# Optimization experiments

Hardware: AMD Instinct MI355X
Metric: run time of the kernel (lower is better)

The kernel has to match this reference:

```python
import jax, jax.numpy as jnp
import numpy as np

# --- static CT geometry (shapes must be static under jit; mirrors the `options` vector) ---
B = 8          # batch
V = 720        # number of projection views
D = 736        # detector bins per view
H = 512        # image height (pixels)
W = 512        # image width  (pixels)
DIMG = 0.006641            # image pixel size (physical units)
DDET = 0.0066              # detector bin size
ANG0 = 0.0                 # starting angle
DANG = 2.0 * np.pi / V     # angular step


def setup_inputs() -> dict:
    key = jax.random.key(0)
    proj = jax.random.normal(key, (B, 1, V, D), dtype=jnp.float32)
    options = jnp.array(
        [V, D, W, H, DIMG, DDET, ANG0, DANG, 5.95, 4.906, 0.0, 2.0],
        dtype=jnp.float32,
    )
    return {"proj": proj, "options": options}


def _backproject(sino):
    """Pixel-driven parallel-beam back-projection of one sinogram [V, D] -> image [H, W]."""
    xs = (jnp.arange(W, dtype=jnp.float32) - (W - 1) / 2.0) * DIMG   # pixel-center x
    ys = ((H - 1) / 2.0 - jnp.arange(H, dtype=jnp.float32)) * DIMG   # pixel-center y
    x = jnp.broadcast_to(xs[None, :], (H, W))
    y = jnp.broadcast_to(ys[:, None], (H, W))
    angles = ANG0 + jnp.arange(V, dtype=jnp.float32) * DANG

    def body(acc, inp):
        ang, row = inp                               # row: [D] detector samples at this view
        t = x * jnp.cos(ang) + y * jnp.sin(ang)      # ray coordinate of each pixel
        u = t / DDET + (D - 1) / 2.0                 # fractional detector index
        u0 = jnp.floor(u)
        w = u - u0
        i0 = u0.astype(jnp.int32)
        i1 = i0 + 1
        v0 = jnp.where((i0 >= 0) & (i0 < D), row[jnp.clip(i0, 0, D - 1)], 0.0)
        v1 = jnp.where((i1 >= 0) & (i1 < D), row[jnp.clip(i1, 0, D - 1)], 0.0)
        return acc + (1.0 - w) * v0 + w * v1, None

    acc, _ = jax.lax.scan(body, jnp.zeros((H, W), jnp.float32), (angles, sino))
    return acc * DANG  # angular integration weight


def reference(proj, options):
    # `options` carries the geometry; its shape-determining entries are baked in statically.
    sino = proj.reshape(B, V, D)
    img = jax.vmap(_backproject)(sino)
    return img.reshape(B, 1, H, W)
```

## Files before the change

### kernel.cpp

```cpp
#include <hip/hip_runtime.h>

#define BATCH 8
#define NVIEW 720
#define NPAIR 360
#define NGRP  180
#define NDET  736
#define IMGH  512
#define IMGW  512

#define DANG_F  ((float)(6.283185307179586 / 720.0))
#define RATIO_F ((float)(0.006641 / 0.0066))
#define UCENTER ((float)((NDET - 1) * 0.5))

#define PADDET 768
#define NITER  90
#define ITER_BYTES 12288
#define WS_BYTES ((size_t)BATCH * NITER * PADDET * 16)

typedef float  v2f __attribute__((ext_vector_type(2)));
typedef __fp16 v2h __attribute__((ext_vector_type(2)));
typedef __fp16 v8h __attribute__((ext_vector_type(8)));

struct alignas(16) E16 { v2h ag, bg, am, bm; };

__device__ __forceinline__ void fuse5(const float* __restrict__ fwd,
                                      const float* __restrict__ rev,
                                      int i, float s[5]) {
    const float4 f4 = *(const float4*)(fwd + i);
    const float  f1 = fwd[i + 4];
    const float4 r4 = *(const float4*)(rev + (732 - i));
    const float  r1 = rev[731 - i];
    s[0] = f4.x + r4.w; s[1] = f4.y + r4.z; s[2] = f4.z + r4.y;
    s[3] = f4.w + r4.x; s[4] = f1 + r1;
}

__global__ __launch_bounds__(192) void prep_kernel(
    const float* __restrict__ proj, E16* __restrict__ ws)
{
    const int t = threadIdx.x;
    if (t >= 184) return;
    const int p = blockIdx.x;
    const int b = blockIdx.y;
    const int g = (p < 89) ? p + 1   : 0;
    const int m = (p < 89) ? 179 - p : 90;
    const int i = 4 * t;
    const float* __restrict__ base = proj + (size_t)b * NVIEW * NDET;
    float sAg[5], sBg[5], sAm[5], sBm[5];
    fuse5(base + (size_t)g * NDET,         base + (size_t)(g + 360) * NDET, i, sAg);
    fuse5(base + (size_t)(g + 180) * NDET, base + (size_t)(g + 540) * NDET, i, sBg);
    fuse5(base + (size_t)m * NDET,         base + (size_t)(m + 360) * NDET, i, sAm);
    fuse5(base + (size_t)(m + 180) * NDET, base + (size_t)(m + 540) * NDET, i, sBm);
    E16* __restrict__ dst = ws + ((size_t)b * NITER + p) * PADDET + i;
#pragma unroll
    for (int k = 0; k < 4; ++k) {
        E16 e;
        e.ag = __builtin_amdgcn_cvt_pkrtz(sAg[k + 1] - sAg[k], sAg[k]);
        e.bg = __builtin_amdgcn_cvt_pkrtz(sBg[k + 1] - sBg[k], sBg[k]);
        e.am = __builtin_amdgcn_cvt_pkrtz(sAm[k + 1] - sAm[k], sAm[k]);
        e.bm = __builtin_amdgcn_cvt_pkrtz(sBm[k + 1] - sBm[k], sBm[k]);
        dst[k] = e;
    }
}

#define VIS(Lp, u, r0, r1, r2, r3) do {                                      \
    const float uu_ = (u);                                                   \
    const int   ii_ = (int)uu_;                                              \
    const v2h wv_ = __builtin_amdgcn_cvt_pkrtz(                              \
        __builtin_amdgcn_fractf(uu_), 1.0f);                                 \
    const v8h E_ = (Lp)[ii_];                                                \
    r0 = __builtin_amdgcn_fdot2((v2h){E_[0], E_[1]}, wv_, r0, false);        \
    r1 = __builtin_amdgcn_fdot2((v2h){E_[2], E_[3]}, wv_, r1, false);        \
    r2 = __builtin_amdgcn_fdot2((v2h){E_[4], E_[5]}, wv_, r2, false);        \
    r3 = __builtin_amdgcn_fdot2((v2h){E_[6], E_[7]}, wv_, r3, false);        \
} while (0)

#define VIS2(Lp, O, u, p0, p1, q0, q1) do {                                  \
    const float uu_ = (u);                                                   \
    const int   ii_ = (int)uu_;                                              \
    const v2h wv_ = __builtin_amdgcn_cvt_pkrtz(                              \
        __builtin_amdgcn_fractf(uu_), 1.0f);                                 \
    const v8h E_ = (Lp)[ii_];                                                \
    const v2h ha_ = {E_[(O)], E_[(O) + 1]};                                  \
    const v2h hb_ = {E_[(O) + 2], E_[(O) + 3]};                              \
    p0 = __builtin_amdgcn_fdot2(ha_, wv_, p0, false);                        \
    p1 = __builtin_amdgcn_fdot2(ha_, wv_, p1, false);                        \
    q0 = __builtin_amdgcn_fdot2(hb_, wv_, q0, false);                        \
    q1 = __builtin_amdgcn_fdot2(hb_, wv_, q1, false);                        \
} while (0)

#define VIS1(Lp, O, u, p0, q0) do {                                          \
    const float uu_ = (u);                                                   \
    const int   ii_ = (int)uu_;                                              \
    const v2h wv_ = __builtin_amdgcn_cvt_pkrtz(                              \
        __builtin_amdgcn_fractf(uu_), 1.0f);                                 \
    const v8h E_ = (Lp)[ii_];                                                \
    p0 = __builtin_amdgcn_fdot2((v2h){E_[(O)], E_[(O) + 1]}, wv_, p0, false);\
    q0 = __builtin_amdgcn_fdot2((v2h){E_[(O) + 2], E_[(O) + 3]}, wv_, q0,    \
                                false);                                      \
} while (0)

__global__ __launch_bounds__(512, 4) void backproject_dma_kernel(
    const v8h* __restrict__ ws, float* __restrict__ out)
{
    __shared__ alignas(16) v8h lds4[4][PADDET];
    __shared__ v2f cs[NGRP];

    const int tid  = threadIdx.x;
    const int wave = tid >> 6;
    const int lane = tid & 63;

    if (tid < NGRP) {
        float s, c;
        sincosf((float)tid * DANG_F, &s, &c);
        cs[tid] = (v2f){c * RATIO_F, s * RATIO_F};
    }

    const int b = blockIdx.z;
    const int h = (int)blockIdx.y * 8 + wave;
    const int w = (int)blockIdx.x * 64 + lane;

    const bool dg = (w == h);
    const bool rm = (w > h);
    const int  H  = rm ? 255 - h : h;
    const int  W  = rm ? 255 - w : w;

    const float px  = (float)W - 255.5f;
    const float py  = 255.5f - (float)H;
    const float px2 = dg ? (-0.5f - (float)W) : py;
    const float py2 = dg ? ( 0.5f + (float)H) : px;

    const char* __restrict__ wsb =
        (const char*)(ws + (size_t)b * NITER * PADDET);

    float A0 = 0.f, A1 = 0.f, A2 = 0.f, A3 = 0.f;
    float B0 = 0.f, B1 = 0.f, B2 = 0.f, B3 = 0.f;
    float X0 = 0.f, X1 = 0.f, X2 = 0.f, X3 = 0.f;
    float Y0 = 0.f, Y1 = 0.f, Y2 = 0.f, Y3 = 0.f;

    auto issue = [&](int p) {
        const char* g0 = wsb + (size_t)p * ITER_BYTES;
        char* l0 = (char*)&lds4[p & 3][0];
        __builtin_amdgcn_global_load_lds(
            (const __attribute__((address_space(1))) void*)
                (g0 + wave * 1024 + lane * 16),
            (__attribute__((address_space(3))) void*)(l0 + wave * 1024),
            16, 0, 0);
        if (wave < 4) {
            const int s = 8 + wave;
            __builtin_amdgcn_global_load_lds(
                (const __attribute__((address_space(1))) void*)
                    (g0 + s * 1024 + lane * 16),
                (__attribute__((address_space(3))) void*)(l0 + s * 1024),
                16, 0, 0);
        }
    };

    issue(0);
    __syncthreads();

    const v2f cc = {UCENTER, UCENTER};
    for (int p = 0; p < NITER - 1; ++p) {
        issue(p + 1);
        {
            const v8h* __restrict__ L = &lds4[p & 3][0];
            const v2f t  = cs[p + 1];
            const v2f m1 = {t.x, -t.y};
            const v2f m2 = {t.y, t.x};
            const v2f gA = __builtin_elementwise_fma(
                (v2f){px, px}, m1, (v2f){py, py} * m2);
            const v2f gB = __builtin_elementwise_fma(
                (v2f){px2, px2}, m1, (v2f){py2, py2} * m2);
            const v2f upA = cc + gA, umA = cc - gA;
            const v2f upB = cc + gB, umB = cc - gB;
            VIS(L, upA.x, A0, A1, X2, X3);
            VIS(L, umA.x, A2, A3, X0, X1);
            VIS(L, upA.y, A3, A0, X3, X0);
            VIS(L, umA.y, A1, A2, X1, X2);
            VIS(L, upB.x, B2, B3, Y0, Y1);
            VIS(L, umB.x, B0, B1, Y2, Y3);
            VIS(L, upB.y, B1, B2, Y1, Y2);
            VIS(L, umB.y, B3, B0, Y3, Y0);
        }
        __syncthreads();
    }

    {
        const v8h* __restrict__ L = &lds4[(NITER - 1) & 3][0];
        const v2f t0 = cs[0], t45 = cs[90];
        if (!dg) {
            const float g1 = px * t0.x + py * t0.y;
            const float g2 = -px * t0.y + py * t0.x;
            VIS2(L, 0, UCENTER + g1, A0, X1, A1, X2);
            VIS2(L, 0, UCENTER - g1, A2, X3, A3, X0);
            VIS2(L, 0, UCENTER + g2, A3, X2, A0, X3);
            VIS2(L, 0, UCENTER - g2, A1, X0, A2, X1);
            const float h1 = px * t45.x + py * t45.y;
            const float h2 = -px * t45.y + py * t45.x;
            VIS2(L, 4, UCENTER + h1, A0, X2, A1, X3);
            VIS2(L, 4, UCENTER - h1, A2, X0, A3, X1);
            VIS2(L, 4, UCENTER + h2, A3, X3, A0, X0);
            VIS2(L, 4, UCENTER - h2, A1, X1, A2, X2);
        } else {
            const float g1  = px * t0.x + py * t0.y;
            const float g1b = px2 * t0.x + py2 * t0.y;
            VIS2(L, 0, UCENTER + g1,  A0, A1, A1, A2);
            VIS2(L, 0, UCENTER - g1,  A2, A3, A0, A3);
            VIS2(L, 0, UCENTER + g1b, B2, B3, B3, B0);
            VIS2(L, 0, UCENTER - g1b, B0, B1, B2, B1);
            {
                const v2h wv_ = __builtin_amdgcn_cvt_pkrtz(0.5f, 1.0f);
                const v8h E_ = L[(int)UCENTER];
                const v2h ha_ = {E_[4], E_[5]};
                const v2h hb_ = {E_[6], E_[7]};
                A0 = __builtin_amdgcn_fdot2(ha_, wv_, A0, false);
                A2 = __builtin_amdgcn_fdot2(ha_, wv_, A2, false);
                B2 = __builtin_amdgcn_fdot2(ha_, wv_, B2, false);
                B0 = __builtin_amdgcn_fdot2(ha_, wv_, B0, false);
                A1 = __builtin_amdgcn_fdot2(hb_, wv_, A1, false);
                A3 = __builtin_amdgcn_fdot2(hb_, wv_, A3, false);
                B3 = __builtin_amdgcn_fdot2(hb_, wv_, B3, false);
                B1 = __builtin_amdgcn_fdot2(hb_, wv_, B1, false);
            }
            const float e1 = (px + px) * t45.x;
            const float e2 = (px2 + px2) * t45.x;
            VIS1(L, 4, UCENTER + e1, A1, A2);
            VIS1(L, 4, UCENTER - e1, A3, A0);
            VIS1(L, 4, UCENTER + e2, B3, B0);
            VIS1(L, 4, UCENTER - e2, B1, B2);
        }
    }

    const float aE0 = dg ? X0 : Y0, aE1 = dg ? X1 : Y1;
    const float aE2 = dg ? X2 : Y2, aE3 = dg ? X3 : Y3;
    const float bE0 = dg ? Y0 : X0, bE1 = dg ? Y1 : X1;
    const float bE2 = dg ? Y2 : X2, bE3 = dg ? Y3 : X3;
    const float a0 = (A0 + aE0) * DANG_F, a1 = (A1 + aE1) * DANG_F;
    const float a2 = (A2 + aE2) * DANG_F, a3 = (A3 + aE3) * DANG_F;
    const float b0 = (B0 + bE0) * DANG_F, b1 = (B1 + bE1) * DANG_F;
    const float b2 = (B2 + bE2) * DANG_F, b3 = (B3 + bE3) * DANG_F;

    float* __restrict__ o = out + (size_t)b * IMGH * IMGW;
    const int Qr = dg ? 256 + H : W;
    const int Qc = dg ? 256 + W : H;
    o[H * IMGW + W]                         = a0;
    o[(511 - W) * IMGW + H]                 = a1;
    o[(511 - H) * IMGW + (511 - W)]         = a2;
    o[W * IMGW + (511 - H)]                 = a3;
    o[Qr * IMGW + Qc]                       = b0;
    o[(511 - Qc) * IMGW + Qr]               = b1;
    o[(511 - Qr) * IMGW + (511 - Qc)]       = b2;
    o[Qc * IMGW + (511 - Qr)]               = b3;
}

struct Stage { float4 f4, r4; float f1, r1; };

__device__ __forceinline__ void fb_load(const float* __restrict__ sino,
                                        int k, int t, Stage& S) {
    if (t < 368) {
        const int p  = (t >= 184);
        const int i  = 4 * (t - 184 * p);
        const int vf = k + 180 * p;
        const float* __restrict__ fwd = sino + vf * NDET;
        const float* __restrict__ rev = sino + (vf + NPAIR) * NDET;
        S.f4 = *(const float4*)(fwd + i);
        S.f1 = fwd[i + 4];
        S.r4 = *(const float4*)(rev + (732 - i));
        S.r1 = rev[731 - i];
    }
}

__device__ __forceinline__ void fb_write(v2h* __restrict__ L, int t,
                                         const Stage& S) {
    if (t < 368) {
        const int p = (t >= 184);
        const int i = 4 * (t - 184 * p);
        const float s0 = S.f4.x + S.r4.w;
        const float s1 = S.f4.y + S.r4.z;
        const float s2 = S.f4.z + S.r4.y;
        const float s3 = S.f4.w + S.r4.x;
        const float s4 = S.f1 + S.r1;
        const v2h n0 = __builtin_amdgcn_cvt_pkrtz(s1 - s0, s0);
        const v2h n1 = __builtin_amdgcn_cvt_pkrtz(s2 - s1, s1);
        const v2h n2 = __builtin_amdgcn_cvt_pkrtz(s3 - s2, s2);
        const v2h n3 = __builtin_amdgcn_cvt_pkrtz(s4 - s3, s3);
        struct alignas(16) H4 { v2h a, b, c, d; };
        *(H4*)(L + p * NDET + i) = H4{n0, n1, n2, n3};
    }
}

__device__ __forceinline__ void fb_visit(const v2h* __restrict__ L,
                                         float u, float& accA, float& accB) {
    const int   i0 = (int)u;
    const float fr = __builtin_amdgcn_fractf(u);
    const v2h wv = __builtin_amdgcn_cvt_pkrtz(fr, 1.0f);
    const v2h A = L[i0];
    const v2h B = L[i0 + NDET];
    accA = __builtin_amdgcn_fdot2(A, wv, accA, false);
    accB = __builtin_amdgcn_fdot2(B, wv, accB, false);
}

__global__ __launch_bounds__(512, 4) void backproject_fb_kernel(
    const float* __restrict__ proj, float* __restrict__ out)
{
    __shared__ alignas(16) v2h lds[2][2][2 * NDET];
    __shared__ v2f cs[NGRP];

    const int tid = threadIdx.x;
    if (tid < NGRP) {
        float s, c;
        sincosf((float)tid * DANG_F, &s, &c);
        cs[tid] = (v2f){c * RATIO_F, s * RATIO_F};
    }

    const int b    = blockIdx.z;
    const int lane = tid & 63;
    const int h    = (int)blockIdx.y * 8 + (tid >> 6);
    const int w0   = (int)blockIdx.x * 64 + lane;

    const float px = (float)w0 - (float)(IMGW - 1) * 0.5f;
    const float py = (float)(IMGH - 1) * 0.5f - (float)h;

    const float* __restrict__ sino = proj + (size_t)b * NVIEW * NDET;

    float a0 = 0.f, a1 = 0.f, a2 = 0.f, a3 = 0.f;
    float b0 = 0.f, b1 = 0.f, b2 = 0.f, b3 = 0.f;

    Stage s0 = {}, s1 = {};
    fb_load(sino, 0, tid, s0);
    fb_load(sino, 1, tid, s1);
    fb_write(lds[0][0], tid, s0);
    fb_write(lds[0][1], tid, s1);
    fb_load(sino, 2, tid, s0);
    fb_load(sino, 3, tid, s1);
    __syncthreads();

    for (int gg = 0; gg < NGRP; gg += 2) {
        const int buf = (gg >> 1) & 1;
#pragma unroll
        for (int sub = 0; sub < 2; ++sub) {
            const v2h* __restrict__ L = lds[buf][sub];
            const v2f t = cs[gg + sub];
            const v2f m1 = {t.x, -t.y};
            const v2f m2 = {t.y, t.x};
            const v2f pxv = {px, px};
            const v2f pyv = {py, py};
            const v2f gvec = __builtin_elementwise_fma(pxv, m1, pyv * m2);
            const v2f cc = {UCENTER, UCENTER};
            const v2f up = cc + gvec;
            const v2f um = cc - gvec;
            const v2f dd = {128.0f, 128.0f};
            const v2f dm = dd * m1;
            const v2f vp = up + dm;
            const v2f vm = um - dm;

            fb_visit(L, up.x, a0, a1);
            fb_visit(L, um.x, a2, a3);
            fb_visit(L, up.y, a3, a0);
            fb_visit(L, um.y, a1, a2);
            fb_visit(L, vp.x, b0, b1);
            fb_visit(L, vm.x, b2, b3);
            fb_visit(L, vp.y, b3, b0);
            fb_visit(L, vm.y, b1, b2);
        }
        if (gg < NGRP - 2) {
            fb_write(lds[buf ^ 1][0], tid, s0);
            fb_write(lds[buf ^ 1][1], tid, s1);
            if (gg < NGRP - 4) {
                fb_load(sino, gg + 4, tid, s0);
                fb_load(sino, gg + 5, tid, s1);
            }
            __syncthreads();
        }
    }

    float* __restrict__ o = out + (size_t)b * IMGH * IMGW;
    const int hm  = (IMGH - 1) - h;
    const int w1  = w0 + 128;
    const int wm0 = (IMGW - 1) - w0;
    const int wm1 = (IMGW - 1) - w1;
    o[h   * IMGW + w0 ] = a0 * DANG_F;
    o[wm0 * IMGW + h  ] = a1 * DANG_F;
    o[hm  * IMGW + wm0] = a2 * DANG_F;
    o[w0  * IMGW + hm ] = a3 * DANG_F;
    o[h   * IMGW + w1 ] = b0 * DANG_F;
    o[wm1 * IMGW + h  ] = b1 * DANG_F;
    o[hm  * IMGW + wm1] = b2 * DANG_F;
    o[w1  * IMGW + hm ] = b3 * DANG_F;
}

extern "C" void kernel_launch(void* const* d_in, const int* in_sizes, int n_in,
                              void* d_out, int out_size, void* d_ws, size_t ws_size,
                              hipStream_t stream) {
    const float* proj = (const float*)d_in[0];
    float* out = (float*)d_out;

    if (ws_size >= WS_BYTES) {
        E16* ws = (E16*)d_ws;
        prep_kernel<<<dim3(NITER, BATCH), 192, 0, stream>>>(proj, ws);
        backproject_dma_kernel<<<dim3(2, 32, BATCH), 512, 0, stream>>>(
            (const v8h*)ws, out);
    } else {
        backproject_fb_kernel<<<dim3(2, 32, BATCH), 512, 0, stream>>>(proj, out);
    }
}
```

Baseline: 144.7 us.

## Swizzle LDS detector layout, interleave batch in block order, double-step DMA loop

Stores the preprocessed detector entries in an XOR-swizzled order so that gathered LDS reads from neighbouring pixels fall into different banks, with the swizzle applied in both the prep writes and every LDS lookup. Block indices are remapped so that consecutive blocks walk across batch images instead of tiles, changing L2 and cache locality. The main loop now processes two angle groups per barrier and issues two DMA prefetches ahead, halving the number of __syncthreads. The added index arithmetic and deeper prefetch use extra VALU work and depend on the 4-slot LDS ring staying consistent.

```diff
diff --git a/kernel.cpp b/kernel.cpp
--- a/kernel.cpp
+++ b/kernel.cpp
@@ -16,6 +16,8 @@
 #define NITER  90
 #define ITER_BYTES 12288
 #define WS_BYTES ((size_t)BATCH * NITER * PADDET * 16)
+
+#define SWZ(j) ((j) ^ (((j) >> 3) & 7))
 
 typedef float  v2f __attribute__((ext_vector_type(2)));
 typedef __fp16 v2h __attribute__((ext_vector_type(2)));
@@ -39,8 +41,9 @@
 {
     const int t = threadIdx.x;
     if (t >= 184) return;
-    const int p = blockIdx.x;
-    const int b = blockIdx.y;
+    const int flat = (int)blockIdx.y * 90 + (int)blockIdx.x;
+    const int b = flat & 7;
+    const int p = flat >> 3;
     const int g = (p < 89) ? p + 1   : 0;
     const int m = (p < 89) ? 179 - p : 90;
     const int i = 4 * t;
@@ -50,7 +53,7 @@
     fuse5(base + (size_t)(g + 180) * NDET, base + (size_t)(g + 540) * NDET, i, sBg);
     fuse5(base + (size_t)m * NDET,         base + (size_t)(m + 360) * NDET, i, sAm);
     fuse5(base + (size_t)(m + 180) * NDET, base + (size_t)(m + 540) * NDET, i, sBm);
-    E16* __restrict__ dst = ws + ((size_t)b * NITER + p) * PADDET + i;
+    E16* __restrict__ dstb = ws + ((size_t)b * NITER + p) * PADDET;
 #pragma unroll
     for (int k = 0; k < 4; ++k) {
         E16 e;
@@ -58,7 +61,8 @@
         e.bg = __builtin_amdgcn_cvt_pkrtz(sBg[k + 1] - sBg[k], sBg[k]);
         e.am = __builtin_amdgcn_cvt_pkrtz(sAm[k + 1] - sAm[k], sAm[k]);
         e.bm = __builtin_amdgcn_cvt_pkrtz(sBm[k + 1] - sBm[k], sBm[k]);
-        dst[k] = e;
+        const int j = i + k;
+        dstb[SWZ(j)] = e;
     }
 }
 
@@ -67,7 +71,7 @@
     const int   ii_ = (int)uu_;                                              \
     const v2h wv_ = __builtin_amdgcn_cvt_pkrtz(                              \
         __builtin_amdgcn_fractf(uu_), 1.0f);                                 \
-    const v8h E_ = (Lp)[ii_];                                                \
+    const v8h E_ = (Lp)[SWZ(ii_)];                                           \
     r0 = __builtin_amdgcn_fdot2((v2h){E_[0], E_[1]}, wv_, r0, false);        \
     r1 = __builtin_amdgcn_fdot2((v2h){E_[2], E_[3]}, wv_, r1, false);        \
     r2 = __builtin_amdgcn_fdot2((v2h){E_[4], E_[5]}, wv_, r2, false);        \
@@ -79,7 +83,7 @@
     const int   ii_ = (int)uu_;                                              \
     const v2h wv_ = __builtin_amdgcn_cvt_pkrtz(                              \
         __builtin_amdgcn_fractf(uu_), 1.0f);                                 \
-    const v8h E_ = (Lp)[ii_];                                                \
+    const v8h E_ = (Lp)[SWZ(ii_)];                                           \
     const v2h ha_ = {E_[(O)], E_[(O) + 1]};                                  \
     const v2h hb_ = {E_[(O) + 2], E_[(O) + 3]};                              \
     p0 = __builtin_amdgcn_fdot2(ha_, wv_, p0, false);                        \
@@ -93,7 +97,7 @@
     const int   ii_ = (int)uu_;                                              \
     const v2h wv_ = __builtin_amdgcn_cvt_pkrtz(                              \
         __builtin_amdgcn_fractf(uu_), 1.0f);                                 \
-    const v8h E_ = (Lp)[ii_];                                                \
+    const v8h E_ = (Lp)[SWZ(ii_)];                                           \
     p0 = __builtin_amdgcn_fdot2((v2h){E_[(O)], E_[(O) + 1]}, wv_, p0, false);\
     q0 = __builtin_amdgcn_fdot2((v2h){E_[(O) + 2], E_[(O) + 3]}, wv_, q0,    \
                                 false);                                      \
@@ -115,9 +119,12 @@
         cs[tid] = (v2f){c * RATIO_F, s * RATIO_F};
     }
 
-    const int b = blockIdx.z;
-    const int h = (int)blockIdx.y * 8 + wave;
-    const int w = (int)blockIdx.x * 64 + lane;
+    const int flat = ((int)blockIdx.z * 32 + (int)blockIdx.y) * 2
+                     + (int)blockIdx.x;
+    const int b    = flat & 7;
+    const int tile = flat >> 3;
+    const int h = (tile >> 1) * 8 + wave;
+    const int w = (tile & 1) * 64 + lane;
 
     const bool dg = (w == h);
     const bool rm = (w > h);
@@ -155,37 +162,43 @@
         }
     };
 
+    const v2f cc = {UCENTER, UCENTER};
+    auto groups = [&](int p) {
+        const v8h* __restrict__ L = &lds4[p & 3][0];
+        const v2f t  = cs[p + 1];
+        const v2f m1 = {t.x, -t.y};
+        const v2f m2 = {t.y, t.x};
+        const v2f gA = __builtin_elementwise_fma(
+            (v2f){px, px}, m1, (v2f){py, py} * m2);
+        const v2f gB = __builtin_elementwise_fma(
+            (v2f){px2, px2}, m1, (v2f){py2, py2} * m2);
+        const v2f upA = cc + gA, umA = cc - gA;
+        const v2f upB = cc + gB, umB = cc - gB;
+        VIS(L, upA.x, A0, A1, X2, X3);
+        VIS(L, umA.x, A2, A3, X0, X1);
+        VIS(L, upA.y, A3, A0, X3, X0);
+        VIS(L, umA.y, A1, A2, X1, X2);
+        VIS(L, upB.x, B2, B3, Y0, Y1);
+        VIS(L, umB.x, B0, B1, Y2, Y3);
+        VIS(L, upB.y, B1, B2, Y1, Y2);
+        VIS(L, umB.y, B3, B0, Y3, Y0);
+    };
+
     issue(0);
+    issue(1);
     __syncthreads();
 
-    const v2f cc = {UCENTER, UCENTER};
-    for (int p = 0; p < NITER - 1; ++p) {
-        issue(p + 1);
-        {
-            const v8h* __restrict__ L = &lds4[p & 3][0];
-            const v2f t  = cs[p + 1];
-            const v2f m1 = {t.x, -t.y};
-            const v2f m2 = {t.y, t.x};
-            const v2f gA = __builtin_elementwise_fma(
-                (v2f){px, px}, m1, (v2f){py, py} * m2);
-            const v2f gB = __builtin_elementwise_fma(
-                (v2f){px2, px2}, m1, (v2f){py2, py2} * m2);
-            const v2f upA = cc + gA, umA = cc - gA;
-            const v2f upB = cc + gB, umB = cc - gB;
-            VIS(L, upA.x, A0, A1, X2, X3);
-            VIS(L, umA.x, A2, A3, X0, X1);
-            VIS(L, upA.y, A3, A0, X3, X0);
-            VIS(L, umA.y, A1, A2, X1, X2);
-            VIS(L, upB.x, B2, B3, Y0, Y1);
-            VIS(L, umB.x, B0, B1, Y2, Y3);
-            VIS(L, upB.y, B1, B2, Y1, Y2);
-            VIS(L, umB.y, B3, B0, Y3, Y0);
-        }
+    for (int k = 0; k < 44; ++k) {
+        issue(2 * k + 2);
+        issue(2 * k + 3);
+        groups(2 * k);
+        groups(2 * k + 1);
         __syncthreads();
     }
+    groups(88);
 
     {
-        const v8h* __restrict__ L = &lds4[(NITER - 1) & 3][0];
+        const v8h* __restrict__ L = &lds4[1][0];
         const v2f t0 = cs[0], t45 = cs[90];
         if (!dg) {
             const float g1 = px * t0.x + py * t0.y;
@@ -209,7 +222,7 @@
             VIS2(L, 0, UCENTER - g1b, B0, B1, B2, B1);
             {
                 const v2h wv_ = __builtin_amdgcn_cvt_pkrtz(0.5f, 1.0f);
-                const v8h E_ = L[(int)UCENTER];
+                const v8h E_ = L[SWZ(367)];
                 const v2h ha_ = {E_[4], E_[5]};
                 const v2h hb_ = {E_[6], E_[7]};
                 A0 = __builtin_amdgcn_fdot2(ha_, wv_, A0, false);
@@ -396,7 +409,7 @@
 
     if (ws_size >= WS_BYTES) {
         E16* ws = (E16*)d_ws;
-        prep_kernel<<<dim3(NITER, BATCH), 192, 0, stream>>>(proj, ws);
+        prep_kernel<<<dim3(90, BATCH), 192, 0, stream>>>(proj, ws);
         backproject_dma_kernel<<<dim3(2, 32, BATCH), 512, 0, stream>>>(
             (const v8h*)ws, out);
     } else {
```

After: 144.6 us. Within noise of the previous version (-0.1%).
